# Kernel tuning notes

Measured on AMD Instinct MI355X. Metric: run time of the kernel, lower is better.

## Reference

```python
import jax, jax.numpy as jnp
import numpy as np
import math

EPS = 1e-07
ALPHA = 0.2
FINAL_LAMBDA = 0.01   # final_beta in the original
ITERATIONS = 2
MEAN_DATA = 1.0

B, H, W, KH, KW, I, O, A = 16, 6, 6, 3, 3, 32, 32, 4


def setup_inputs() -> dict:
    key = jax.random.key(0)
    k1, k2 = jax.random.split(key)
    votes = jax.random.normal(k1, (B, H, W, KH, KW, I, O, A, A), dtype=jnp.float32)
    activations = jax.random.uniform(k2, (B, H, W, KH, KW, I, 1, 1, 1), dtype=jnp.float32)
    beta_a = jnp.full((1, 1, 1, 1, 1, 1, O, 1, 1), 0.5, dtype=jnp.float32)
    beta_u = jnp.full((1, 1, 1, 1, 1, 1, O, 1, 1), 0.5, dtype=jnp.float32)
    return {"votes": votes, "activations": activations, "beta_a": beta_a, "beta_u": beta_u}


def _m_step(a_i, V, R, R_prev, beta_a, beta_u, it_idx):
    # R mixing with previous assignments (faithful to source)
    R = R * a_i * (1.0 - ALPHA) + ALPHA * R_prev
    R_prev = R
    # reduce over kernel (3,4) and input-capsule (5) axes
    sum_R = jnp.sum(R, axis=(3, 4, 5), keepdims=True)                      # (b,h,w,1,1,1,o,1,1)
    mu = jnp.sum(R * V, axis=(3, 4, 5), keepdims=True) / (sum_R + EPS)     # (b,h,w,1,1,1,o,a,a)
    sigma_sq = jnp.sum(R * (V - mu) ** 2, axis=(3, 4, 5), keepdims=True) / (sum_R + EPS)
    cost_h = (beta_u - 0.5 * jnp.log(sigma_sq + EPS)) * sum_R / MEAN_DATA
    inv_temp = FINAL_LAMBDA * (1.0 - 0.95 ** (it_idx + 1))
    a_j = jax.nn.sigmoid(inv_temp * (beta_a - jnp.sum(cost_h, axis=(-1, -2), keepdims=True)))
    return mu, sigma_sq, a_j, R_prev


def _e_step_log(V, mu, sigma_sq, a_j):
    # log-space E-step: log N(V; mu, sigma) summed over the 4x4 pose entries
    log_p = -jnp.sum(jnp.log(2.0 * math.pi * sigma_sq + EPS) + (V - mu) ** 2 / (2.0 * sigma_sq),
                     axis=(-1, -2), keepdims=True)                         # (b,h,w,kh,kw,i,o,1,1)
    log_num = jnp.log(a_j + EPS) + log_p
    log_den = jax.scipy.special.logsumexp(log_num, axis=(3, 4, 6), keepdims=True)
    return jnp.exp(log_num - log_den)


def reference(votes, activations, beta_a, beta_u):
    b, h, w, kh, kw, i, o, a, _ = votes.shape
    # softmax over zeros along axis 6 -> uniform 1/o
    R = jnp.full((b, h, w, 1, 1, i, o, 1, 1), 1.0 / o, dtype=votes.dtype)
    R_prev = R
    mu = sigma_sq = a_j = None
    for it in range(ITERATIONS - 1):
        mu, sigma_sq, a_j, R_prev = _m_step(activations, votes, R, R_prev, beta_a, beta_u, it)
        R = _e_step_log(votes, mu, sigma_sq, a_j)
    # final M-step called with i = iterations (matches source)
    mu, sigma_sq, a_j, R_prev = _m_step(activations, votes, R, R_prev, beta_a, beta_u, ITERATIONS)
    poses = jnp.squeeze(mu, axis=(3, 4, 5))   # (b,h,w,o,a,a)
    acts = jnp.squeeze(a_j, axis=(3, 4, 5))   # (b,h,w,o,1,1)
    return poses, acts
```

## Files before the change

kernel.cpp:

```cpp
#include <hip/hip_runtime.h>


#define KKc 9
#define NIc 32
#define NOc 32
#define NAc 16
#define KIc 288
#define NPc 512
#define NSITE 576
#define RSTR 20

#define EPSf 1e-7f
#define TWO_PIf 6.28318530717958647692f

__device__ __forceinline__ float wave_sum(float v) {
#pragma unroll
  for (int off = 32; off; off >>= 1) v += __shfl_down(v, off, 64);
  return v;
}
__device__ __forceinline__ float wave_max(float v) {
#pragma unroll
  for (int off = 32; off; off >>= 1) v = fmaxf(v, __shfl_down(v, off, 64));
  return v;
}

__global__ __launch_bounds__(128)
void em_k1(const float* __restrict__ votes, const float* __restrict__ acts_in,
           const float* __restrict__ beta_a, const float* __restrict__ beta_u,
           float* __restrict__ w_mu1, float* __restrict__ w_i2s,
           float* __restrict__ w_m1v, float* __restrict__ w_m1q,
           float* __restrict__ w_base, float* __restrict__ w_sR1)
{
  const int site = blockIdx.x >> 2;
  const int qtr  = blockIdx.x & 3;
  const int t    = threadIdx.x;

  __shared__ float s_act[KIc];
  __shared__ float s_red[2];
  __shared__ float s_cr[32 * 9];

  s_act[t] = acts_in[site * KIc + t];
  s_act[t + 128] = acts_in[site * KIc + t + 128];
  if (t < 32) s_act[t + 256] = acts_in[site * KIc + t + 256];
  __syncthreads();

  float v = fmaf(0.8f, s_act[t], 0.2f) + fmaf(0.8f, s_act[t + 128], 0.2f);
  if (t < 32) v += fmaf(0.8f, s_act[t + 256], 0.2f);
  v = wave_sum(v);
  if ((t & 63) == 0) s_red[t >> 6] = v;
  __syncthreads();
  const float sumR1 = (s_red[0] + s_red[1]) * 0.03125f;

  const int c  = qtr * 32 + (t & 31);
  const int r0 = t >> 5;
  float pv0 = 0.f, pv1 = 0.f, pv2 = 0.f, pv3 = 0.f;
  float pq0 = 0.f, pq1 = 0.f, pq2 = 0.f, pq3 = 0.f;
  const float4* vb = reinterpret_cast<const float4*>(votes) + (size_t)site * (KIc * 128) + c;
#pragma unroll 8
  for (int k = 0; k < 72; ++k) {
    const int ki = r0 + 4 * k;
    const float r = fmaf(0.8f, s_act[ki], 0.2f) * 0.03125f;
    const float4 x = vb[(size_t)ki * 128];
    pv0 = fmaf(r, x.x, pv0); pq0 = fmaf(r, x.x * x.x, pq0);
    pv1 = fmaf(r, x.y, pv1); pq1 = fmaf(r, x.y * x.y, pq1);
    pv2 = fmaf(r, x.z, pv2); pq2 = fmaf(r, x.z * x.z, pq2);
    pv3 = fmaf(r, x.w, pv3); pq3 = fmaf(r, x.w * x.w, pq3);
  }
  pv0 += __shfl_xor(pv0, 32); pv1 += __shfl_xor(pv1, 32);
  pv2 += __shfl_xor(pv2, 32); pv3 += __shfl_xor(pv3, 32);
  pq0 += __shfl_xor(pq0, 32); pq1 += __shfl_xor(pq1, 32);
  pq2 += __shfl_xor(pq2, 32); pq3 += __shfl_xor(pq3, 32);
  if (t >= 64 && t < 96) {
    const int l = t - 64;
    s_cr[l * 9 + 0] = pv0; s_cr[l * 9 + 1] = pv1; s_cr[l * 9 + 2] = pv2; s_cr[l * 9 + 3] = pv3;
    s_cr[l * 9 + 4] = pq0; s_cr[l * 9 + 5] = pq1; s_cr[l * 9 + 6] = pq2; s_cr[l * 9 + 7] = pq3;
  }
  __syncthreads();
  if (t < 32) {
    pv0 += s_cr[t * 9 + 0]; pv1 += s_cr[t * 9 + 1]; pv2 += s_cr[t * 9 + 2]; pv3 += s_cr[t * 9 + 3];
    pq0 += s_cr[t * 9 + 4]; pq1 += s_cr[t * 9 + 5]; pq2 += s_cr[t * 9 + 6]; pq3 += s_cr[t * 9 + 7];

    const float sR1e = sumR1 + EPSf;
    const float sR1x = sumR1 + 2.f * EPSf;
    const float mu0 = pv0 / sR1e, mu1 = pv1 / sR1e, mu2 = pv2 / sR1e, mu3 = pv3 / sR1e;
    const float sg0 = fmaxf((pq0 - mu0 * mu0 * sR1x) / sR1e, 0.f);
    const float sg1 = fmaxf((pq1 - mu1 * mu1 * sR1x) / sR1e, 0.f);
    const float sg2 = fmaxf((pq2 - mu2 * mu2 * sR1x) / sR1e, 0.f);
    const float sg3 = fmaxf((pq3 - mu3 * mu3 * sR1x) / sR1e, 0.f);

    const size_t fo = (size_t)site * 128 + c;
    reinterpret_cast<float4*>(w_mu1)[fo] = make_float4(mu0, mu1, mu2, mu3);
    reinterpret_cast<float4*>(w_i2s)[fo] = make_float4(0.5f / sg0, 0.5f / sg1, 0.5f / sg2, 0.5f / sg3);
    reinterpret_cast<float4*>(w_m1v)[fo] = make_float4(pv0, pv1, pv2, pv3);
    reinterpret_cast<float4*>(w_m1q)[fo] = make_float4(pq0, pq1, pq2, pq3);

    const int o = c >> 2;
    const float bu = beta_u[o];
    float lt = logf(TWO_PIf * sg0 + EPSf) + logf(TWO_PIf * sg1 + EPSf)
             + logf(TWO_PIf * sg2 + EPSf) + logf(TWO_PIf * sg3 + EPSf);
    float ch = (4.f * bu - 0.5f * (logf(sg0 + EPSf) + logf(sg1 + EPSf)
                                 + logf(sg2 + EPSf) + logf(sg3 + EPSf))) * sumR1;
    ch += __shfl_xor(ch, 1); ch += __shfl_xor(ch, 2);
    lt += __shfl_xor(lt, 1); lt += __shfl_xor(lt, 2);
    if ((t & 3) == 0) {
      const float aj = 1.f / (1.f + expf(-(0.0005f * (beta_a[o] - ch))));
      w_base[site * NOc + o] = logf(aj + EPSf) - lt;
    }
    if (t == 0) w_sR1[site] = sumR1;
  }
}

__global__ __launch_bounds__(256)
void em_k3(const float* __restrict__ votes, const float* __restrict__ acts_in,
           const float* __restrict__ w_mu1, const float* __restrict__ w_i2s,
           const float* __restrict__ w_base, float* __restrict__ w_part)
{
  const int site = (NSITE - 1) - (blockIdx.x >> 3);
  const int ig   = blockIdx.x & 7;
  const int t    = threadIdx.x;
  const int o    = t & 31;

  __shared__ float s_V[288 * RSTR];
  __shared__ float s_act[KIc];
  __shared__ float s_base[NOc];
  __shared__ float s_rm[4];
  __shared__ float s_re[4];

  {
    const int tt = t & 127;
    const float4 x = reinterpret_cast<const float4*>((t < 128 ? w_mu1 : w_i2s) + (size_t)site * NPc)[tt];
    float* dst = s_V + (t < 128 ? 0 : 544) + (tt >> 2) * 17 + (tt & 3) * 4;
    dst[0] = x.x; dst[1] = x.y; dst[2] = x.z; dst[3] = x.w;
  }
  s_act[t] = acts_in[site * KIc + t];
  if (t < 32) { s_act[256 + t] = acts_in[site * KIc + 256 + t]; s_base[t] = w_base[site * NOc + t]; }
  __syncthreads();
  float mu[16], is[16];
#pragma unroll
  for (int a = 0; a < 16; ++a) { mu[a] = s_V[o * 17 + a]; is[a] = s_V[544 + o * 17 + a]; }
  const float lbase = s_base[o];
  __syncthreads();

  float accv[16], accq[16], accw = 0.f;
#pragma unroll
  for (int a = 0; a < 16; ++a) { accv[a] = 0.f; accq[a] = 0.f; }

  const float4* vsl4 = reinterpret_cast<const float4*>(votes) + (size_t)site * (KIc * 128);

  for (int ii = 0; ii < 4; ++ii) {
    const int i = ig * 4 + ii;
#pragma unroll
    for (int idx = t; idx < 1152; idx += 256) {
      const int row = idx >> 2;
      const int a4  = idx & 3;
      const float4 x = vsl4[(size_t)((row >> 5) * NIc + i) * 128 + (row & 31) * 4 + a4];
      *reinterpret_cast<float4*>(s_V + row * RSTR + a4 * 4) = x;
    }
    __syncthreads();

    float v1[16];
#pragma unroll
    for (int j = 0; j < 4; ++j) {
      const float4 x = *reinterpret_cast<const float4*>(s_V + t * RSTR + 4 * j);
      v1[4 * j] = x.x; v1[4 * j + 1] = x.y; v1[4 * j + 2] = x.z; v1[4 * j + 3] = x.w;
    }
    float lp1 = 0.f;
#pragma unroll
    for (int a = 0; a < 16; ++a) { const float d = v1[a] - mu[a]; lp1 = fmaf(d * d, is[a], lp1); }
    const float ln1 = lbase - lp1;

    float v2[16];
    float ln2 = -1e30f;
    if (t < 32) {
#pragma unroll
      for (int j = 0; j < 4; ++j) {
        const float4 x = *reinterpret_cast<const float4*>(s_V + (256 + t) * RSTR + 4 * j);
        v2[4 * j] = x.x; v2[4 * j + 1] = x.y; v2[4 * j + 2] = x.z; v2[4 * j + 3] = x.w;
      }
      float lp2 = 0.f;
#pragma unroll
      for (int a = 0; a < 16; ++a) { const float d = v2[a] - mu[a]; lp2 = fmaf(d * d, is[a], lp2); }
      ln2 = lbase - lp2;
    }

    float m = wave_max(fmaxf(ln1, ln2));
    if ((t & 63) == 0) s_rm[t >> 6] = m;
    __syncthreads();
    m = fmaxf(fmaxf(s_rm[0], s_rm[1]), fmaxf(s_rm[2], s_rm[3]));
    float e = expf(ln1 - m) + ((t < 32) ? expf(ln2 - m) : 0.f);
    e = wave_sum(e);
    if ((t & 63) == 0) s_re[t >> 6] = e;
    __syncthreads();
    const float logden = m + logf(s_re[0] + s_re[1] + s_re[2] + s_re[3]);

    const float w1 = expf(ln1 - logden) * s_act[(t >> 5) * NIc + i] * 0.8f;
    accw += w1;
#pragma unroll
    for (int a = 0; a < 16; ++a) {
      accv[a] = fmaf(w1, v1[a], accv[a]);
      accq[a] = fmaf(w1, v1[a] * v1[a], accq[a]);
    }
    if (t < 32) {
      const float w2 = expf(ln2 - logden) * s_act[8 * NIc + i] * 0.8f;
      accw += w2;
#pragma unroll
      for (int a = 0; a < 16; ++a) {
        accv[a] = fmaf(w2, v2[a], accv[a]);
        accq[a] = fmaf(w2, v2[a] * v2[a], accq[a]);
      }
    }
  }

  accw += __shfl_xor(accw, 32);
#pragma unroll
  for (int a = 0; a < 16; ++a) {
    accv[a] += __shfl_xor(accv[a], 32);
    accq[a] += __shfl_xor(accq[a], 32);
  }
  float* s_p = s_V;
  {
    const int l = t & 63, wv = t >> 6;
    if (l < 32) {
#pragma unroll
      for (int a = 0; a < 16; ++a) {
        s_p[a * 128 + wv * 32 + l] = accv[a];
        s_p[(16 + a) * 128 + wv * 32 + l] = accq[a];
      }
      s_p[32 * 128 + wv * 32 + l] = accw;
    }
  }
  __syncthreads();
  float* wp = w_part + (size_t)(site * 8 + ig) * (33 * 32);
  for (int j = t >> 5; j < 33; j += 8) {
    const float s = s_p[j * 128 + o] + s_p[j * 128 + 32 + o]
                  + s_p[j * 128 + 64 + o] + s_p[j * 128 + 96 + o];
    wp[j * 32 + o] = s;
  }
}

__global__ __launch_bounds__(256)
void em_k4(const float* __restrict__ beta_a, const float* __restrict__ beta_u,
           const float* __restrict__ w_m1v, const float* __restrict__ w_m1q,
           const float* __restrict__ w_sR1, const float* __restrict__ w_part,
           float* __restrict__ out)
{
  const int site = blockIdx.x;
  const int t    = threadIdx.x;
  const int oB   = t & 31;
  const int a2B  = (t >> 5) * 2;

  __shared__ float s_M[33 * 32];
  __shared__ float s_c[256];

  for (int j = t >> 5; j < 33; j += 8) {
    float s = 0.f;
#pragma unroll
    for (int g = 0; g < 8; ++g)
      s += w_part[(size_t)(site * 8 + g) * (33 * 32) + j * 32 + oB];
    s_M[j * 32 + oB] = s;
  }
  __syncthreads();

  const float sumR1 = w_sR1[site];
  const float sumR  = s_M[32 * 32 + oB] + 0.2f * sumR1;
  const float sRe   = sumR + EPSf;
  const float sRx   = sumR + 2.f * EPSf;
  const int p = oB * NAc + a2B;

  const float Mva = s_M[a2B * 32 + oB]        + 0.2f * w_m1v[(size_t)site * NPc + p];
  const float Mvb = s_M[(a2B + 1) * 32 + oB]  + 0.2f * w_m1v[(size_t)site * NPc + p + 1];
  const float Mqa = s_M[(16 + a2B) * 32 + oB] + 0.2f * w_m1q[(size_t)site * NPc + p];
  const float Mqb = s_M[(17 + a2B) * 32 + oB] + 0.2f * w_m1q[(size_t)site * NPc + p + 1];

  const float mua = Mva / sRe;
  const float mub = Mvb / sRe;
  const float sga = fmaxf((Mqa - mua * mua * sRx) / sRe, 0.f);
  const float sgb = fmaxf((Mqb - mub * mub * sRx) / sRe, 0.f);

  reinterpret_cast<float2*>(out + (size_t)site * NPc)[p >> 1] = make_float2(mua, mub);

  const float bu = beta_u[oB];
  s_c[t] = (bu - 0.5f * logf(sga + EPSf)) * sumR
         + (bu - 0.5f * logf(sgb + EPSf)) * sumR;
  __syncthreads();
  if (t < NOc) {
    float c = 0.f;
#pragma unroll
    for (int k = 0; k < 8; ++k) c += s_c[t + 32 * k];
    const float aj = 1.f / (1.f + expf(-(0.00142625f * (beta_a[t] - c))));
    out[(size_t)NSITE * NPc + site * NOc + t] = aj;
  }
}

extern "C" void kernel_launch(void* const* d_in, const int* in_sizes, int n_in,
                              void* d_out, int out_size, void* d_ws, size_t ws_size,
                              hipStream_t stream) {
  const float* votes  = (const float*)d_in[0];
  const float* acts   = (const float*)d_in[1];
  const float* beta_a = (const float*)d_in[2];
  const float* beta_u = (const float*)d_in[3];
  float* out = (float*)d_out;

  float* ws = (float*)d_ws;
  const size_t SP = (size_t)NSITE * NPc;
  float* w_mu1  = ws;
  float* w_i2s  = ws + SP;
  float* w_m1v  = ws + 2 * SP;
  float* w_m1q  = ws + 3 * SP;
  float* w_base = ws + 4 * SP;
  float* w_sR1  = w_base + NSITE * NOc;
  float* w_part = w_sR1 + 1024;

  em_k1<<<NSITE * 4, 128, 0, stream>>>(votes, acts, beta_a, beta_u,
                                       w_mu1, w_i2s, w_m1v, w_m1q, w_base, w_sR1);
  em_k3<<<NSITE * 8, 256, 0, stream>>>(votes, acts, w_mu1, w_i2s, w_base, w_part);
  em_k4<<<NSITE, 256, 0, stream>>>(beta_a, beta_u, w_m1v, w_m1q, w_sR1, w_part, out);
}
```

Baseline: 554.6 us.

## Fuse three EM routing kernels into one per-site kernel

Merges the first M-step, the E-step plus second M-step accumulation, and the final reduction into a single kernel with one block per site. Intermediates (mu, inverse sigma, partial sums) stay in shared memory instead of workspace, and the E-step now reads votes straight from global memory with per-wave reductions instead of staging them in LDS. This removes two launches and the workspace round-trips. In exchange there are only 576 blocks, so fewer parallel blocks are available to hide latency, and votes are re-read from global memory in the E-step.

```diff
diff --git a/kernel.cpp b/kernel.cpp
--- a/kernel.cpp
+++ b/kernel.cpp
@@ -8,278 +8,199 @@
 #define KIc 288
 #define NPc 512
 #define NSITE 576
-#define RSTR 20
-
 #define EPSf 1e-7f
 #define TWO_PIf 6.28318530717958647692f
 
-__device__ __forceinline__ float wave_sum(float v) {
-#pragma unroll
-  for (int off = 32; off; off >>= 1) v += __shfl_down(v, off, 64);
-  return v;
-}
-__device__ __forceinline__ float wave_max(float v) {
-#pragma unroll
-  for (int off = 32; off; off >>= 1) v = fmaxf(v, __shfl_down(v, off, 64));
-  return v;
-}
-
-__global__ __launch_bounds__(128)
-void em_k1(const float* __restrict__ votes, const float* __restrict__ acts_in,
-           const float* __restrict__ beta_a, const float* __restrict__ beta_u,
-           float* __restrict__ w_mu1, float* __restrict__ w_i2s,
-           float* __restrict__ w_m1v, float* __restrict__ w_m1q,
-           float* __restrict__ w_base, float* __restrict__ w_sR1)
-{
-  const int site = blockIdx.x >> 2;
-  const int qtr  = blockIdx.x & 3;
-  const int t    = threadIdx.x;
-
-  __shared__ float s_act[KIc];
-  __shared__ float s_red[2];
-  __shared__ float s_cr[32 * 9];
-
-  s_act[t] = acts_in[site * KIc + t];
-  s_act[t + 128] = acts_in[site * KIc + t + 128];
-  if (t < 32) s_act[t + 256] = acts_in[site * KIc + t + 256];
-  __syncthreads();
-
-  float v = fmaf(0.8f, s_act[t], 0.2f) + fmaf(0.8f, s_act[t + 128], 0.2f);
-  if (t < 32) v += fmaf(0.8f, s_act[t + 256], 0.2f);
-  v = wave_sum(v);
-  if ((t & 63) == 0) s_red[t >> 6] = v;
-  __syncthreads();
-  const float sumR1 = (s_red[0] + s_red[1]) * 0.03125f;
-
-  const int c  = qtr * 32 + (t & 31);
-  const int r0 = t >> 5;
-  float pv0 = 0.f, pv1 = 0.f, pv2 = 0.f, pv3 = 0.f;
-  float pq0 = 0.f, pq1 = 0.f, pq2 = 0.f, pq3 = 0.f;
-  const float4* vb = reinterpret_cast<const float4*>(votes) + (size_t)site * (KIc * 128) + c;
-#pragma unroll 8
-  for (int k = 0; k < 72; ++k) {
-    const int ki = r0 + 4 * k;
-    const float r = fmaf(0.8f, s_act[ki], 0.2f) * 0.03125f;
-    const float4 x = vb[(size_t)ki * 128];
-    pv0 = fmaf(r, x.x, pv0); pq0 = fmaf(r, x.x * x.x, pq0);
-    pv1 = fmaf(r, x.y, pv1); pq1 = fmaf(r, x.y * x.y, pq1);
-    pv2 = fmaf(r, x.z, pv2); pq2 = fmaf(r, x.z * x.z, pq2);
-    pv3 = fmaf(r, x.w, pv3); pq3 = fmaf(r, x.w * x.w, pq3);
-  }
-  pv0 += __shfl_xor(pv0, 32); pv1 += __shfl_xor(pv1, 32);
-  pv2 += __shfl_xor(pv2, 32); pv3 += __shfl_xor(pv3, 32);
-  pq0 += __shfl_xor(pq0, 32); pq1 += __shfl_xor(pq1, 32);
-  pq2 += __shfl_xor(pq2, 32); pq3 += __shfl_xor(pq3, 32);
-  if (t >= 64 && t < 96) {
-    const int l = t - 64;
-    s_cr[l * 9 + 0] = pv0; s_cr[l * 9 + 1] = pv1; s_cr[l * 9 + 2] = pv2; s_cr[l * 9 + 3] = pv3;
-    s_cr[l * 9 + 4] = pq0; s_cr[l * 9 + 5] = pq1; s_cr[l * 9 + 6] = pq2; s_cr[l * 9 + 7] = pq3;
-  }
-  __syncthreads();
-  if (t < 32) {
-    pv0 += s_cr[t * 9 + 0]; pv1 += s_cr[t * 9 + 1]; pv2 += s_cr[t * 9 + 2]; pv3 += s_cr[t * 9 + 3];
-    pq0 += s_cr[t * 9 + 4]; pq1 += s_cr[t * 9 + 5]; pq2 += s_cr[t * 9 + 6]; pq3 += s_cr[t * 9 + 7];
-
-    const float sR1e = sumR1 + EPSf;
-    const float sR1x = sumR1 + 2.f * EPSf;
-    const float mu0 = pv0 / sR1e, mu1 = pv1 / sR1e, mu2 = pv2 / sR1e, mu3 = pv3 / sR1e;
-    const float sg0 = fmaxf((pq0 - mu0 * mu0 * sR1x) / sR1e, 0.f);
-    const float sg1 = fmaxf((pq1 - mu1 * mu1 * sR1x) / sR1e, 0.f);
-    const float sg2 = fmaxf((pq2 - mu2 * mu2 * sR1x) / sR1e, 0.f);
-    const float sg3 = fmaxf((pq3 - mu3 * mu3 * sR1x) / sR1e, 0.f);
-
-    const size_t fo = (size_t)site * 128 + c;
-    reinterpret_cast<float4*>(w_mu1)[fo] = make_float4(mu0, mu1, mu2, mu3);
-    reinterpret_cast<float4*>(w_i2s)[fo] = make_float4(0.5f / sg0, 0.5f / sg1, 0.5f / sg2, 0.5f / sg3);
-    reinterpret_cast<float4*>(w_m1v)[fo] = make_float4(pv0, pv1, pv2, pv3);
-    reinterpret_cast<float4*>(w_m1q)[fo] = make_float4(pq0, pq1, pq2, pq3);
-
-    const int o = c >> 2;
-    const float bu = beta_u[o];
-    float lt = logf(TWO_PIf * sg0 + EPSf) + logf(TWO_PIf * sg1 + EPSf)
-             + logf(TWO_PIf * sg2 + EPSf) + logf(TWO_PIf * sg3 + EPSf);
-    float ch = (4.f * bu - 0.5f * (logf(sg0 + EPSf) + logf(sg1 + EPSf)
-                                 + logf(sg2 + EPSf) + logf(sg3 + EPSf))) * sumR1;
-    ch += __shfl_xor(ch, 1); ch += __shfl_xor(ch, 2);
-    lt += __shfl_xor(lt, 1); lt += __shfl_xor(lt, 2);
-    if ((t & 3) == 0) {
-      const float aj = 1.f / (1.f + expf(-(0.0005f * (beta_a[o] - ch))));
-      w_base[site * NOc + o] = logf(aj + EPSf) - lt;
-    }
-    if (t == 0) w_sR1[site] = sumR1;
-  }
-}
-
-__global__ __launch_bounds__(256)
-void em_k3(const float* __restrict__ votes, const float* __restrict__ acts_in,
-           const float* __restrict__ w_mu1, const float* __restrict__ w_i2s,
-           const float* __restrict__ w_base, float* __restrict__ w_part)
-{
-  const int site = (NSITE - 1) - (blockIdx.x >> 3);
-  const int ig   = blockIdx.x & 7;
-  const int t    = threadIdx.x;
-  const int o    = t & 31;
-
-  __shared__ float s_V[288 * RSTR];
-  __shared__ float s_act[KIc];
-  __shared__ float s_base[NOc];
-  __shared__ float s_rm[4];
-  __shared__ float s_re[4];
-
-  {
-    const int tt = t & 127;
-    const float4 x = reinterpret_cast<const float4*>((t < 128 ? w_mu1 : w_i2s) + (size_t)site * NPc)[tt];
-    float* dst = s_V + (t < 128 ? 0 : 544) + (tt >> 2) * 17 + (tt & 3) * 4;
-    dst[0] = x.x; dst[1] = x.y; dst[2] = x.z; dst[3] = x.w;
-  }
-  s_act[t] = acts_in[site * KIc + t];
-  if (t < 32) { s_act[256 + t] = acts_in[site * KIc + 256 + t]; s_base[t] = w_base[site * NOc + t]; }
-  __syncthreads();
-  float mu[16], is[16];
-#pragma unroll
-  for (int a = 0; a < 16; ++a) { mu[a] = s_V[o * 17 + a]; is[a] = s_V[544 + o * 17 + a]; }
-  const float lbase = s_base[o];
-  __syncthreads();
-
-  float accv[16], accq[16], accw = 0.f;
-#pragma unroll
-  for (int a = 0; a < 16; ++a) { accv[a] = 0.f; accq[a] = 0.f; }
-
-  const float4* vsl4 = reinterpret_cast<const float4*>(votes) + (size_t)site * (KIc * 128);
-
-  for (int ii = 0; ii < 4; ++ii) {
-    const int i = ig * 4 + ii;
-#pragma unroll
-    for (int idx = t; idx < 1152; idx += 256) {
-      const int row = idx >> 2;
-      const int a4  = idx & 3;
-      const float4 x = vsl4[(size_t)((row >> 5) * NIc + i) * 128 + (row & 31) * 4 + a4];
-      *reinterpret_cast<float4*>(s_V + row * RSTR + a4 * 4) = x;
-    }
-    __syncthreads();
-
-    float v1[16];
-#pragma unroll
-    for (int j = 0; j < 4; ++j) {
-      const float4 x = *reinterpret_cast<const float4*>(s_V + t * RSTR + 4 * j);
-      v1[4 * j] = x.x; v1[4 * j + 1] = x.y; v1[4 * j + 2] = x.z; v1[4 * j + 3] = x.w;
-    }
-    float lp1 = 0.f;
-#pragma unroll
-    for (int a = 0; a < 16; ++a) { const float d = v1[a] - mu[a]; lp1 = fmaf(d * d, is[a], lp1); }
-    const float ln1 = lbase - lp1;
-
-    float v2[16];
-    float ln2 = -1e30f;
-    if (t < 32) {
-#pragma unroll
-      for (int j = 0; j < 4; ++j) {
-        const float4 x = *reinterpret_cast<const float4*>(s_V + (256 + t) * RSTR + 4 * j);
-        v2[4 * j] = x.x; v2[4 * j + 1] = x.y; v2[4 * j + 2] = x.z; v2[4 * j + 3] = x.w;
-      }
-      float lp2 = 0.f;
-#pragma unroll
-      for (int a = 0; a < 16; ++a) { const float d = v2[a] - mu[a]; lp2 = fmaf(d * d, is[a], lp2); }
-      ln2 = lbase - lp2;
-    }
-
-    float m = wave_max(fmaxf(ln1, ln2));
-    if ((t & 63) == 0) s_rm[t >> 6] = m;
-    __syncthreads();
-    m = fmaxf(fmaxf(s_rm[0], s_rm[1]), fmaxf(s_rm[2], s_rm[3]));
-    float e = expf(ln1 - m) + ((t < 32) ? expf(ln2 - m) : 0.f);
-    e = wave_sum(e);
-    if ((t & 63) == 0) s_re[t >> 6] = e;
-    __syncthreads();
-    const float logden = m + logf(s_re[0] + s_re[1] + s_re[2] + s_re[3]);
-
-    const float w1 = expf(ln1 - logden) * s_act[(t >> 5) * NIc + i] * 0.8f;
-    accw += w1;
-#pragma unroll
-    for (int a = 0; a < 16; ++a) {
-      accv[a] = fmaf(w1, v1[a], accv[a]);
-      accq[a] = fmaf(w1, v1[a] * v1[a], accq[a]);
-    }
-    if (t < 32) {
-      const float w2 = expf(ln2 - logden) * s_act[8 * NIc + i] * 0.8f;
-      accw += w2;
-#pragma unroll
-      for (int a = 0; a < 16; ++a) {
-        accv[a] = fmaf(w2, v2[a], accv[a]);
-        accq[a] = fmaf(w2, v2[a] * v2[a], accq[a]);
-      }
-    }
-  }
-
-  accw += __shfl_xor(accw, 32);
-#pragma unroll
-  for (int a = 0; a < 16; ++a) {
-    accv[a] += __shfl_xor(accv[a], 32);
-    accq[a] += __shfl_xor(accq[a], 32);
-  }
-  float* s_p = s_V;
-  {
-    const int l = t & 63, wv = t >> 6;
-    if (l < 32) {
-#pragma unroll
-      for (int a = 0; a < 16; ++a) {
-        s_p[a * 128 + wv * 32 + l] = accv[a];
-        s_p[(16 + a) * 128 + wv * 32 + l] = accq[a];
-      }
-      s_p[32 * 128 + wv * 32 + l] = accw;
-    }
-  }
-  __syncthreads();
-  float* wp = w_part + (size_t)(site * 8 + ig) * (33 * 32);
-  for (int j = t >> 5; j < 33; j += 8) {
-    const float s = s_p[j * 128 + o] + s_p[j * 128 + 32 + o]
-                  + s_p[j * 128 + 64 + o] + s_p[j * 128 + 96 + o];
-    wp[j * 32 + o] = s;
-  }
-}
-
-__global__ __launch_bounds__(256)
-void em_k4(const float* __restrict__ beta_a, const float* __restrict__ beta_u,
-           const float* __restrict__ w_m1v, const float* __restrict__ w_m1q,
-           const float* __restrict__ w_sR1, const float* __restrict__ w_part,
-           float* __restrict__ out)
+__global__ __launch_bounds__(256, 3)
+void em_fused(const float* __restrict__ votes, const float* __restrict__ acts_in,
+              const float* __restrict__ beta_a, const float* __restrict__ beta_u,
+              float* __restrict__ out)
 {
   const int site = blockIdx.x;
   const int t    = threadIdx.x;
-  const int oB   = t & 31;
-  const int a2B  = (t >> 5) * 2;
-
-  __shared__ float s_M[33 * 32];
-  __shared__ float s_c[256];
-
-  for (int j = t >> 5; j < 33; j += 8) {
-    float s = 0.f;
-#pragma unroll
-    for (int g = 0; g < 8; ++g)
-      s += w_part[(size_t)(site * 8 + g) * (33 * 32) + j * 32 + oB];
-    s_M[j * 32 + oB] = s;
-  }
-  __syncthreads();
-
-  const float sumR1 = w_sR1[site];
-  const float sumR  = s_M[32 * 32 + oB] + 0.2f * sumR1;
-  const float sRe   = sumR + EPSf;
-  const float sRx   = sumR + 2.f * EPSf;
+
+  __shared__ float s_act[KIc];
+  __shared__ float s_mu[NPc];
+  __shared__ float s_is[NPc];
+  __shared__ float s_m1v[NPc];
+  __shared__ float s_m1q[NPc];
+  __shared__ float s_base[NOc];
+  __shared__ float s_red[4];
+  __shared__ float s_scr[4224 + 1056];
+
+  s_act[t] = acts_in[site * KIc + t];
+  if (t < 32) s_act[256 + t] = acts_in[site * KIc + 256 + t];
+  __syncthreads();
+  {
+    float v = fmaf(0.8f, s_act[t], 0.2f);
+    if (t < 32) v += fmaf(0.8f, s_act[256 + t], 0.2f);
+#pragma unroll
+    for (int off = 32; off; off >>= 1) v += __shfl_down(v, off, 64);
+    if ((t & 63) == 0) s_red[t >> 6] = v;
+  }
+  __syncthreads();
+  const float sumR1 = (s_red[0] + s_red[1] + s_red[2] + s_red[3]) * 0.03125f;
+
+  {
+    const int c  = t & 127;
+    const int rr = t >> 7;
+    const float4* vb = reinterpret_cast<const float4*>(votes) + (size_t)site * (KIc * 128) + c;
+    float pv0 = 0.f, pv1 = 0.f, pv2 = 0.f, pv3 = 0.f;
+    float pq0 = 0.f, pq1 = 0.f, pq2 = 0.f, pq3 = 0.f;
+#pragma unroll 8
+    for (int k = 0; k < 144; ++k) {
+      const int ki = rr + 2 * k;
+      const float r = fmaf(0.8f, s_act[ki], 0.2f) * 0.03125f;
+      const float4 x = vb[(size_t)ki * 128];
+      pv0 = fmaf(r, x.x, pv0); pq0 = fmaf(r, x.x * x.x, pq0);
+      pv1 = fmaf(r, x.y, pv1); pq1 = fmaf(r, x.y * x.y, pq1);
+      pv2 = fmaf(r, x.z, pv2); pq2 = fmaf(r, x.z * x.z, pq2);
+      pv3 = fmaf(r, x.w, pv3); pq3 = fmaf(r, x.w * x.w, pq3);
+    }
+    if (t >= 128) {
+      float* f = s_scr + (size_t)(t - 128) * 8;
+      f[0] = pv0; f[1] = pv1; f[2] = pv2; f[3] = pv3;
+      f[4] = pq0; f[5] = pq1; f[6] = pq2; f[7] = pq3;
+    }
+    __syncthreads();
+    if (t < 128) {
+      const float* f = s_scr + (size_t)t * 8;
+      pv0 += f[0]; pv1 += f[1]; pv2 += f[2]; pv3 += f[3];
+      pq0 += f[4]; pq1 += f[5]; pq2 += f[6]; pq3 += f[7];
+
+      const float sR1e = sumR1 + EPSf, sR1x = sumR1 + 2.f * EPSf;
+      const float mu0 = pv0 / sR1e, mu1 = pv1 / sR1e, mu2 = pv2 / sR1e, mu3 = pv3 / sR1e;
+      const float sg0 = fmaxf((pq0 - mu0 * mu0 * sR1x) / sR1e, 0.f);
+      const float sg1 = fmaxf((pq1 - mu1 * mu1 * sR1x) / sR1e, 0.f);
+      const float sg2 = fmaxf((pq2 - mu2 * mu2 * sR1x) / sR1e, 0.f);
+      const float sg3 = fmaxf((pq3 - mu3 * mu3 * sR1x) / sR1e, 0.f);
+
+      const int b = t * 4;
+      s_mu[b] = mu0; s_mu[b + 1] = mu1; s_mu[b + 2] = mu2; s_mu[b + 3] = mu3;
+      s_is[b] = 0.5f / sg0; s_is[b + 1] = 0.5f / sg1; s_is[b + 2] = 0.5f / sg2; s_is[b + 3] = 0.5f / sg3;
+      s_m1v[b] = pv0; s_m1v[b + 1] = pv1; s_m1v[b + 2] = pv2; s_m1v[b + 3] = pv3;
+      s_m1q[b] = pq0; s_m1q[b + 1] = pq1; s_m1q[b + 2] = pq2; s_m1q[b + 3] = pq3;
+
+      const int o = t >> 2;
+      const float bu = beta_u[o];
+      float lt = logf(TWO_PIf * sg0 + EPSf) + logf(TWO_PIf * sg1 + EPSf)
+               + logf(TWO_PIf * sg2 + EPSf) + logf(TWO_PIf * sg3 + EPSf);
+      float ch = (4.f * bu - 0.5f * (logf(sg0 + EPSf) + logf(sg1 + EPSf)
+                                   + logf(sg2 + EPSf) + logf(sg3 + EPSf))) * sumR1;
+      ch += __shfl_xor(ch, 1, 64); ch += __shfl_xor(ch, 2, 64);
+      lt += __shfl_xor(lt, 1, 64); lt += __shfl_xor(lt, 2, 64);
+      if ((t & 3) == 0) {
+        const float aj = 1.f / (1.f + expf(-(0.0005f * (beta_a[o] - ch))));
+        s_base[o] = logf(aj + EPSf) - lt;
+      }
+    }
+    __syncthreads();
+  }
+
+  const int wv = t >> 6, l = t & 63, o = l & 31, h = l >> 5;
+  float mu[16], is[16];
+#pragma unroll
+  for (int a = 0; a < 16; ++a) { mu[a] = s_mu[o * 16 + a]; is[a] = s_is[o * 16 + a]; }
+  const float lbase = s_base[o];
+  const bool  v5    = (h == 0);
+
+  float accv[16], accq[16], accw = 0.f;
+#pragma unroll
+  for (int a = 0; a < 16; ++a) { accv[a] = 0.f; accq[a] = 0.f; }
+
+  const float* vsb = votes + (size_t)site * (KIc * NPc) + o * NAc;
+
+  for (int jj = 0; jj < 8; ++jj) {
+    const int i = wv * 8 + jj;
+    float lp[5];
+#pragma unroll
+    for (int r = 0; r < 5; ++r) {
+      const int kk = (r < 4) ? (h + 2 * r) : 8;
+      const float4* p4 = reinterpret_cast<const float4*>(vsb + (size_t)(kk * NIc + i) * NPc);
+      float acc = 0.f;
+#pragma unroll
+      for (int j = 0; j < 4; ++j) {
+        const float4 x = p4[j];
+        float d;
+        d = x.x - mu[4 * j];     acc = fmaf(d * d, is[4 * j],     acc);
+        d = x.y - mu[4 * j + 1]; acc = fmaf(d * d, is[4 * j + 1], acc);
+        d = x.z - mu[4 * j + 2]; acc = fmaf(d * d, is[4 * j + 2], acc);
+        d = x.w - mu[4 * j + 3]; acc = fmaf(d * d, is[4 * j + 3], acc);
+      }
+      lp[r] = acc;
+    }
+    float mn = fminf(fminf(lp[0], lp[1]), fminf(lp[2], lp[3]));
+    if (v5) mn = fminf(mn, lp[4]);
+    float lnx = lbase - mn;
+#pragma unroll
+    for (int off = 32; off; off >>= 1) lnx = fmaxf(lnx, __shfl_xor(lnx, off, 64));
+    float e = expf(lbase - lp[0] - lnx) + expf(lbase - lp[1] - lnx)
+            + expf(lbase - lp[2] - lnx) + expf(lbase - lp[3] - lnx);
+    if (v5) e += expf(lbase - lp[4] - lnx);
+#pragma unroll
+    for (int off = 32; off; off >>= 1) e += __shfl_xor(e, off, 64);
+    const float logden = lnx + logf(e);
+    const float sb = lbase - logden;
+
+#pragma unroll
+    for (int r = 0; r < 5; ++r) {
+      const int kk = (r < 4) ? (h + 2 * r) : 8;
+      float w = expf(sb - lp[r]) * (s_act[kk * NIc + i] * 0.8f);
+      if (r == 4 && !v5) w = 0.f;
+      accw += w;
+      const float4* p4 = reinterpret_cast<const float4*>(vsb + (size_t)(kk * NIc + i) * NPc);
+#pragma unroll
+      for (int j = 0; j < 4; ++j) {
+        const float4 x = p4[j];
+        accv[4 * j]     = fmaf(w, x.x, accv[4 * j]);     accq[4 * j]     = fmaf(w, x.x * x.x, accq[4 * j]);
+        accv[4 * j + 1] = fmaf(w, x.y, accv[4 * j + 1]); accq[4 * j + 1] = fmaf(w, x.y * x.y, accq[4 * j + 1]);
+        accv[4 * j + 2] = fmaf(w, x.z, accv[4 * j + 2]); accq[4 * j + 2] = fmaf(w, x.z * x.z, accq[4 * j + 2]);
+        accv[4 * j + 3] = fmaf(w, x.w, accv[4 * j + 3]); accq[4 * j + 3] = fmaf(w, x.w * x.w, accq[4 * j + 3]);
+      }
+    }
+  }
+
+  accw += __shfl_xor(accw, 32, 64);
+#pragma unroll
+  for (int a = 0; a < 16; ++a) {
+    accv[a] += __shfl_xor(accv[a], 32, 64);
+    accq[a] += __shfl_xor(accq[a], 32, 64);
+  }
+  float* s_p = s_scr;
+  if (l < 32) {
+#pragma unroll
+    for (int a = 0; a < 16; ++a) {
+      s_p[a * 128 + wv * 32 + l]        = accv[a];
+      s_p[(16 + a) * 128 + wv * 32 + l] = accq[a];
+    }
+    s_p[32 * 128 + wv * 32 + l] = accw;
+  }
+  __syncthreads();
+  float* s_M = s_scr + 4224;
+  {
+    const int oo = t & 31;
+    for (int j = t >> 5; j < 33; j += 8)
+      s_M[j * 32 + oo] = s_p[j * 128 + oo] + s_p[j * 128 + 32 + oo]
+                       + s_p[j * 128 + 64 + oo] + s_p[j * 128 + 96 + oo];
+  }
+  __syncthreads();
+
+  const int oB = t & 31, a2B = (t >> 5) * 2;
   const int p = oB * NAc + a2B;
-
-  const float Mva = s_M[a2B * 32 + oB]        + 0.2f * w_m1v[(size_t)site * NPc + p];
-  const float Mvb = s_M[(a2B + 1) * 32 + oB]  + 0.2f * w_m1v[(size_t)site * NPc + p + 1];
-  const float Mqa = s_M[(16 + a2B) * 32 + oB] + 0.2f * w_m1q[(size_t)site * NPc + p];
-  const float Mqb = s_M[(17 + a2B) * 32 + oB] + 0.2f * w_m1q[(size_t)site * NPc + p + 1];
-
-  const float mua = Mva / sRe;
-  const float mub = Mvb / sRe;
+  const float sumR = s_M[32 * 32 + oB] + 0.2f * sumR1;
+  const float sRe = sumR + EPSf, sRx = sumR + 2.f * EPSf;
+  const float Mva = s_M[a2B * 32 + oB]        + 0.2f * s_m1v[p];
+  const float Mvb = s_M[(a2B + 1) * 32 + oB]  + 0.2f * s_m1v[p + 1];
+  const float Mqa = s_M[(16 + a2B) * 32 + oB] + 0.2f * s_m1q[p];
+  const float Mqb = s_M[(17 + a2B) * 32 + oB] + 0.2f * s_m1q[p + 1];
+  const float mua = Mva / sRe, mub = Mvb / sRe;
   const float sga = fmaxf((Mqa - mua * mua * sRx) / sRe, 0.f);
   const float sgb = fmaxf((Mqb - mub * mub * sRx) / sRe, 0.f);
 
   reinterpret_cast<float2*>(out + (size_t)site * NPc)[p >> 1] = make_float2(mua, mub);
 
   const float bu = beta_u[oB];
+  float* s_c = s_scr;
   s_c[t] = (bu - 0.5f * logf(sga + EPSf)) * sumR
          + (bu - 0.5f * logf(sgb + EPSf)) * sumR;
   __syncthreads();
@@ -300,19 +221,5 @@
   const float* beta_a = (const float*)d_in[2];
   const float* beta_u = (const float*)d_in[3];
   float* out = (float*)d_out;
-
-  float* ws = (float*)d_ws;
-  const size_t SP = (size_t)NSITE * NPc;
-  float* w_mu1  = ws;
-  float* w_i2s  = ws + SP;
-  float* w_m1v  = ws + 2 * SP;
-  float* w_m1q  = ws + 3 * SP;
-  float* w_base = ws + 4 * SP;
-  float* w_sR1  = w_base + NSITE * NOc;
-  float* w_part = w_sR1 + 1024;
-
-  em_k1<<<NSITE * 4, 128, 0, stream>>>(votes, acts, beta_a, beta_u,
-                                       w_mu1, w_i2s, w_m1v, w_m1q, w_base, w_sR1);
-  em_k3<<<NSITE * 8, 256, 0, stream>>>(votes, acts, w_mu1, w_i2s, w_base, w_part);
-  em_k4<<<NSITE, 256, 0, stream>>>(beta_a, beta_u, w_m1v, w_m1q, w_sR1, w_part, out);
+  em_fused<<<NSITE, 256, 0, stream>>>(votes, acts, beta_a, beta_u, out);
 }
```

Result: slower. 694.8 us (+25.3%).
